# Optimization experiments

Measured on AMD Instinct MI355X. Metric: run time of the kernel, lower is better.

Reference implementation:

```python
import jax, jax.numpy as jnp
import numpy as np

N_ITEM = 100000
DIV_TRADEOFF = 0.1


def setup_inputs() -> dict:
    key = jax.random.key(0)
    ks = jax.random.split(key, 9)
    B, K, L, D_LLM, H = 512, 8, 50, 768, 128
    return {
        "user_id": jax.random.randint(ks[0], (B,), 0, 50000),
        "base_model_preds": jax.random.randint(ks[1], (B, K, L), 0, N_ITEM + 1),
        "preference_in": jax.random.normal(ks[2], (B, H), jnp.float32),
        "pos_label": jax.random.normal(ks[3], (B, K), jnp.float32),
        "neg_label": jax.random.normal(ks[4], (B, K), jnp.float32),
        "user_embeddings": jax.random.normal(ks[5], (50000, H), jnp.float32) * 0.01,
        "item_embeddings": jax.random.normal(ks[6], (N_ITEM + 1, D_LLM), jnp.float32) * 0.02,
        "W_proj": jax.random.normal(ks[7], (D_LLM, H), jnp.float32) * (1.0 / np.sqrt(D_LLM)),
        "b_proj": jax.random.normal(ks[8], (H,), jnp.float32) * 0.01,
    }


def reference(user_id, base_model_preds, preference_in, pos_label, neg_label,
              user_embeddings, item_embeddings, W_proj, b_proj):
    B, K, L = base_model_preds.shape
    # masked gather-embed: ids outside (0, n_item] map to a zero row
    valid = (base_model_preds > 0) & (base_model_preds <= N_ITEM)
    safe_ids = jnp.where(valid, base_model_preds, 0)
    focus_llm = item_embeddings[safe_ids] * valid[..., None].astype(item_embeddings.dtype)  # [B,K,L,D_llm]
    # linear projection to hidden (bias applied everywhere, matching nn.Linear on zeroed rows)
    bm = jnp.einsum('bkld,dh->bklh', focus_llm, W_proj) + b_proj  # [B,K,L,H]
    # time-decay weighted sum over sequence positions
    time_w = 1.0 / jnp.log2(jnp.arange(L, dtype=jnp.float32) + 2.0)  # [L]
    basemodel_emb = jnp.einsum('bklh,l->bkh', bm, time_w)  # [B,K,H]
    # preference = DIEN(...) + user_emb  (DIEN output modeled by preference_in)
    preference = preference_in + user_embeddings[user_id]  # [B,H]
    wgts_org = jnp.einsum('bkh,bh->bk', basemodel_emb, preference)
    wgts = jax.nn.softmax(wgts_org, axis=-1)  # [B,K]
    pos_scores = jnp.sum(pos_label * wgts, axis=1)
    neg_scores = jnp.sum(neg_label * wgts, axis=1)
    loss = -jnp.sum(jax.nn.log_sigmoid(pos_scores - neg_scores))
    # diversity regularizer (use_div=True)
    cov_wgt = jax.lax.stop_gradient(wgts[:, None, :] + wgts[:, :, None])  # [B,K,K]
    cov_mask = 1.0 - jnp.eye(K, dtype=wgts.dtype)  # [K,K]
    gram = jnp.einsum('bih,bjh->bij', basemodel_emb, basemodel_emb) ** 2
    loss_div = DIV_TRADEOFF * jnp.mean(cov_mask[None] * gram * cov_wgt)
    return loss + loss_div
```

## Files before the change

### kernel.cpp

```cpp
#include <hip/hip_runtime.h>
#include <math.h>

#define B_SZ 512
#define K_SZ 8
#define L_SZ 50
#define DLLM 768
#define H_SZ 128
#define N_ITEM 100000
#define DIV_TRADEOFF 0.1f
#define M_PAD 100032

typedef float  f32x4 __attribute__((ext_vector_type(4)));
typedef short  bf16x8 __attribute__((ext_vector_type(8)));
typedef unsigned int u32x4 __attribute__((ext_vector_type(4)));
typedef unsigned short u16x8 __attribute__((ext_vector_type(8)));

__device__ __forceinline__ unsigned short f2bf(float f) {
    unsigned u = __float_as_uint(f);
    u += 0x7fffu + ((u >> 16) & 1u);
    return (unsigned short)(u >> 16);
}

__device__ __forceinline__ void gload_lds16(const void* g, void* l) {
    __builtin_amdgcn_global_load_lds(
        (const __attribute__((address_space(1))) unsigned*)g,
        (__attribute__((address_space(3))) unsigned*)l, 16, 0, 0);
}

__global__ __launch_bounds__(256) void k_wt(
    const float* __restrict__ W,
    unsigned short* __restrict__ Wt,
    float* __restrict__ out)
{
    __shared__ float tile[64][65];
    const int kb = blockIdx.x >> 1;
    const int nb = blockIdx.x & 1;
    const int t  = threadIdx.x;
    if (blockIdx.x == 0 && t == 0) out[0] = 0.0f;

    const int r  = t >> 2;
    const int c0 = (t & 3) * 16;
    #pragma unroll
    for (int j = 0; j < 4; ++j) {
        const float4 v = *(const float4*)(W + (size_t)(kb * 64 + r) * H_SZ + nb * 64 + c0 + j * 4);
        tile[r][c0 + j * 4 + 0] = v.x;
        tile[r][c0 + j * 4 + 1] = v.y;
        tile[r][c0 + j * 4 + 2] = v.z;
        tile[r][c0 + j * 4 + 3] = v.w;
    }
    __syncthreads();
    const int n  = t >> 2;
    const int k0 = (t & 3) * 16;
    u16x8 lo, hi;
    #pragma unroll
    for (int j = 0; j < 8; ++j) lo[j] = f2bf(tile[k0 + j][n]);
    #pragma unroll
    for (int j = 0; j < 8; ++j) hi[j] = f2bf(tile[k0 + 8 + j][n]);
    unsigned short* dst = Wt + (size_t)(nb * 64 + n) * DLLM + kb * 64 + k0;
    *(u16x8*)(dst)     = lo;
    *(u16x8*)(dst + 8) = hi;
}

__global__ __launch_bounds__(256) void k_proj(
    const float* __restrict__ item,
    const unsigned short* __restrict__ Wt,
    float* __restrict__ proj)
{
    __shared__ float          As[64 * 64];
    __shared__ unsigned short Bs[128 * 64];

    const int t    = threadIdx.x;
    const int brow = blockIdx.x * 64;
    const int w    = t >> 6;
    const int lane = t & 63;
    const int nl   = lane & 15;
    const int g    = lane >> 4;
    const int key  = nl & 7;

    const int a_rsub = (lane >> 4);
    const int a_gl   = lane & 15;
    const int b_nsub = (lane >> 3);
    const int b_gl   = lane & 7;
    const int b_key  = b_nsub & 7;

    const int r = w * 16 + nl;

    f32x4 acc[8];
    #pragma unroll
    for (int i = 0; i < 8; ++i) acc[i] = (f32x4){0.f, 0.f, 0.f, 0.f};

    for (int c = 0; c < 12; ++c) {
        const int kc = c * 64;

        #pragma unroll
        for (int i = 0; i < 4; ++i) {
            const int row_t = w * 16 + i * 4 + a_rsub;
            const int rowS  = (brow + row_t <= N_ITEM) ? (brow + row_t) : N_ITEM;
            const int ka    = (a_gl ^ (row_t & 7)) * 4;
            gload_lds16(item + (size_t)rowS * DLLM + kc + ka,
                        &As[w * 1024 + i * 256]);
        }
        #pragma unroll
        for (int i = 0; i < 4; ++i) {
            const int n_t = w * 32 + i * 8 + b_nsub;
            const int kb  = (b_gl ^ b_key) * 8;
            gload_lds16(Wt + (size_t)n_t * DLLM + kc + kb,
                        &Bs[w * 2048 + i * 512]);
        }
        __syncthreads();

        #pragma unroll
        for (int ks = 0; ks < 2; ++ks) {
            const f32x4 alo = *(const f32x4*)&As[r * 64 + 4 * ((ks * 8 + 2 * g)     ^ key)];
            const f32x4 ahi = *(const f32x4*)&As[r * 64 + 4 * ((ks * 8 + 2 * g + 1) ^ key)];
            unsigned p0, p1, p2, p3;
            asm("v_cvt_pk_bf16_f32 %0, %1, %2" : "=v"(p0) : "v"(alo.x), "v"(alo.y));
            asm("v_cvt_pk_bf16_f32 %0, %1, %2" : "=v"(p1) : "v"(alo.z), "v"(alo.w));
            asm("v_cvt_pk_bf16_f32 %0, %1, %2" : "=v"(p2) : "v"(ahi.x), "v"(ahi.y));
            asm("v_cvt_pk_bf16_f32 %0, %1, %2" : "=v"(p3) : "v"(ahi.z), "v"(ahi.w));
            union { u32x4 u; bf16x8 s; } af;
            af.u[0] = p0; af.u[1] = p1; af.u[2] = p2; af.u[3] = p3;

            #pragma unroll
            for (int nt = 0; nt < 8; ++nt) {
                const bf16x8 b = *(const bf16x8*)&Bs[(nt * 16 + nl) * 64
                                                     + 8 * ((ks * 4 + g) ^ key)];
                acc[nt] = __builtin_amdgcn_mfma_f32_16x16x32_bf16(af.s, b, acc[nt], 0, 0, 0);
            }
        }
        __syncthreads();
    }

    const int rbase = brow + w * 16 + 4 * g;
    #pragma unroll
    for (int nt = 0; nt < 8; ++nt) {
        #pragma unroll
        for (int rr = 0; rr < 4; ++rr) {
            proj[(size_t)(rbase + rr) * H_SZ + nt * 16 + nl] = acc[nt][rr];
        }
    }
}

__global__ __launch_bounds__(256) void k_gather2(
    const int* __restrict__ preds,
    const float* __restrict__ proj,
    const float* __restrict__ bproj,
    float* __restrict__ emb)
{
    const int tid = threadIdx.x;
    const int sub = tid >> 7;
    const int h   = tid & 127;
    const int bk  = blockIdx.x * 2 + sub;
    const int* __restrict__ p = preds + (size_t)bk * L_SZ;

    constexpr int PF = 8;
    float buf[PF], wgt[PF];
    #pragma unroll
    for (int i = 0; i < PF; ++i) {
        const int id = p[i];
        const bool v = (id > 0) && (id <= N_ITEM);
        wgt[i] = v ? (1.0f / log2f((float)(i + 2))) : 0.0f;
        buf[i] = proj[(size_t)(v ? id : 0) * H_SZ + h];
    }
    float acc = 0.f;
    #pragma unroll
    for (int l = 0; l < L_SZ; ++l) {
        const int s = l % PF;
        acc += wgt[s] * buf[s];
        if (l + PF < L_SZ) {
            const int id = p[l + PF];
            const bool v = (id > 0) && (id <= N_ITEM);
            wgt[s] = v ? (1.0f / log2f((float)(l + PF + 2))) : 0.0f;
            buf[s] = proj[(size_t)(v ? id : 0) * H_SZ + h];
        }
    }
    float sumw = 0.f;
    #pragma unroll
    for (int l = 0; l < L_SZ; ++l) sumw += 1.0f / log2f((float)(l + 2));
    emb[(size_t)bk * H_SZ + h] = acc + bproj[h] * sumw;
}

__global__ __launch_bounds__(256) void k_loss(
    const int* __restrict__ user_id, const float* __restrict__ pref_in,
    const float* __restrict__ pos_label, const float* __restrict__ neg_label,
    const float* __restrict__ user_emb, const float* __restrict__ emb,
    float* __restrict__ out)
{
    const int b = blockIdx.x;
    const int tid = threadIdx.x;
    __shared__ float pref[H_SZ];
    __shared__ float e[K_SZ][H_SZ + 1];
    __shared__ float sdot[K_SZ];
    __shared__ float wg[K_SZ];
    __shared__ float lossb_s;
    if (tid < H_SZ) {
        const int uid = user_id[b];
        pref[tid] = pref_in[(size_t)b * H_SZ + tid] + user_emb[(size_t)uid * H_SZ + tid];
    }
    const float* eb = emb + (size_t)b * K_SZ * H_SZ;
    #pragma unroll
    for (int i = 0; i < 4; ++i) {
        const int idx = tid * 4 + i;
        e[idx >> 7][idx & (H_SZ - 1)] = eb[idx];
    }
    __syncthreads();
    {
        const int k = tid >> 5;
        const int lane = tid & 31;
        float s = e[k][lane] * pref[lane] + e[k][lane + 32] * pref[lane + 32]
                + e[k][lane + 64] * pref[lane + 64] + e[k][lane + 96] * pref[lane + 96];
        #pragma unroll
        for (int m = 16; m >= 1; m >>= 1) s += __shfl_xor(s, m, 64);
        if (lane == 0) sdot[k] = s;
    }
    __syncthreads();
    if (tid == 0) {
        float mx = sdot[0];
        #pragma unroll
        for (int k = 1; k < K_SZ; ++k) mx = fmaxf(mx, sdot[k]);
        float sum = 0.f; float ex[K_SZ];
        #pragma unroll
        for (int k = 0; k < K_SZ; ++k) { ex[k] = expf(sdot[k] - mx); sum += ex[k]; }
        float ps = 0.f, ns = 0.f;
        #pragma unroll
        for (int k = 0; k < K_SZ; ++k) {
            const float w = ex[k] / sum;
            wg[k] = w;
            ps += pos_label[(size_t)b * K_SZ + k] * w;
            ns += neg_label[(size_t)b * K_SZ + k] * w;
        }
        const float x = ps - ns;
        lossb_s = fmaxf(-x, 0.f) + log1pf(expf(-fabsf(x)));
    }
    __syncthreads();
    if (tid < 64) {
        const int i = tid >> 3;
        const int j = tid & 7;
        float g = 0.f;
        for (int h = 0; h < H_SZ; ++h) g += e[i][h] * e[j][h];
        float v = (i != j) ? (g * g * (wg[i] + wg[j])) : 0.f;
        #pragma unroll
        for (int m = 32; m >= 1; m >>= 1) v += __shfl_xor(v, m, 64);
        if (tid == 0) {
            const float mean_div = v / (float)(B_SZ * K_SZ * K_SZ);
            atomicAdd(out, lossb_s + DIV_TRADEOFF * mean_div);
        }
    }
}

__global__ __launch_bounds__(192) void k_gather_fb(
    const int* __restrict__ preds, const float* __restrict__ item,
    float* __restrict__ wf, float* __restrict__ out)
{
    const int bk  = blockIdx.x;
    const int tid = threadIdx.x;
    if (bk == 0 && tid == 0) out[0] = 0.0f;
    const int* __restrict__ p = preds + (size_t)bk * L_SZ;
    const float* __restrict__ ibase = item + (size_t)tid * 4;
    float4 acc = make_float4(0.f, 0.f, 0.f, 0.f);
    constexpr int PF = 8;
    float4 buf[PF]; float wgt[PF];
    #pragma unroll
    for (int i = 0; i < PF; ++i) {
        const int id = p[i];
        const bool v = (id > 0) && (id <= N_ITEM);
        wgt[i] = v ? (1.0f / log2f((float)(i + 2))) : 0.0f;
        buf[i] = *(const float4*)(ibase + (size_t)(v ? id : 0) * DLLM);
    }
    #pragma unroll
    for (int l = 0; l < L_SZ; ++l) {
        const int s = l % PF;
        const float4 v4 = buf[s];
        const float  w  = wgt[s];
        if (l + PF < L_SZ) {
            const int id = p[l + PF];
            const bool v = (id > 0) && (id <= N_ITEM);
            wgt[s] = v ? (1.0f / log2f((float)(l + PF + 2))) : 0.0f;
            buf[s] = *(const float4*)(ibase + (size_t)(v ? id : 0) * DLLM);
        }
        acc.x += w * v4.x; acc.y += w * v4.y; acc.z += w * v4.z; acc.w += w * v4.w;
    }
    *(float4*)(wf + (size_t)bk * DLLM + (size_t)tid * 4) = acc;
}

__global__ __launch_bounds__(256) void k_projloss_fb(
    const float* __restrict__ wf, const float* __restrict__ W,
    const float* __restrict__ bproj, const int* __restrict__ user_id,
    const float* __restrict__ pref_in, const float* __restrict__ pos_label,
    const float* __restrict__ neg_label, const float* __restrict__ user_emb,
    float* __restrict__ out)
{
    const int b   = blockIdx.x;
    const int tid = threadIdx.x;
    const int c   = tid & (H_SZ - 1);
    const int rg  = tid >> 7;
    __shared__ float A[K_SZ][H_SZ];
    __shared__ float e[K_SZ][H_SZ + 1];
    __shared__ float pref[H_SZ];
    __shared__ float sdot[K_SZ];
    __shared__ float wg[K_SZ];
    __shared__ float lossb_s;
    float acc[4] = {0.f, 0.f, 0.f, 0.f};
    const size_t rowbase = (size_t)b * K_SZ;
    for (int kb = 0; kb < DLLM; kb += H_SZ) {
        __syncthreads();
        {
            const int r  = tid >> 5;
            const int kk = (tid & 31) * 4;
            *(float4*)&A[r][kk] = *(const float4*)(wf + (rowbase + r) * DLLM + kb + kk);
        }
        __syncthreads();
        #pragma unroll 4
        for (int k = 0; k < H_SZ; k += 4) {
            const float4 a0 = *(const float4*)&A[rg][k];
            const float4 a1 = *(const float4*)&A[rg + 2][k];
            const float4 a2 = *(const float4*)&A[rg + 4][k];
            const float4 a3 = *(const float4*)&A[rg + 6][k];
            const float* Wp = W + (size_t)(kb + k) * H_SZ + c;
            const float w0 = Wp[0]; const float w1 = Wp[H_SZ];
            const float w2 = Wp[2 * H_SZ]; const float w3 = Wp[3 * H_SZ];
            acc[0] += a0.x * w0 + a0.y * w1 + a0.z * w2 + a0.w * w3;
            acc[1] += a1.x * w0 + a1.y * w1 + a1.z * w2 + a1.w * w3;
            acc[2] += a2.x * w0 + a2.y * w1 + a2.z * w2 + a2.w * w3;
            acc[3] += a3.x * w0 + a3.y * w1 + a3.z * w2 + a3.w * w3;
        }
    }
    float sumw = 0.f;
    #pragma unroll
    for (int l = 0; l < L_SZ; ++l) sumw += 1.0f / log2f((float)(l + 2));
    const float bterm = bproj[c] * sumw;
    #pragma unroll
    for (int ri = 0; ri < 4; ++ri) e[rg + 2 * ri][c] = acc[ri] + bterm;
    if (tid < H_SZ) {
        const int uid = user_id[b];
        pref[tid] = pref_in[(size_t)b * H_SZ + tid] + user_emb[(size_t)uid * H_SZ + tid];
    }
    __syncthreads();
    {
        const int k    = tid >> 5;
        const int lane = tid & 31;
        float s = e[k][lane] * pref[lane] + e[k][lane + 32] * pref[lane + 32]
                + e[k][lane + 64] * pref[lane + 64] + e[k][lane + 96] * pref[lane + 96];
        #pragma unroll
        for (int m = 16; m >= 1; m >>= 1) s += __shfl_xor(s, m, 64);
        if (lane == 0) sdot[k] = s;
    }
    __syncthreads();
    if (tid == 0) {
        float mx = sdot[0];
        #pragma unroll
        for (int k = 1; k < K_SZ; ++k) mx = fmaxf(mx, sdot[k]);
        float sum = 0.f; float ex[K_SZ];
        #pragma unroll
        for (int k = 0; k < K_SZ; ++k) { ex[k] = expf(sdot[k] - mx); sum += ex[k]; }
        float ps = 0.f, ns = 0.f;
        #pragma unroll
        for (int k = 0; k < K_SZ; ++k) {
            const float w = ex[k] / sum;
            wg[k] = w;
            ps += pos_label[(size_t)b * K_SZ + k] * w;
            ns += neg_label[(size_t)b * K_SZ + k] * w;
        }
        const float x = ps - ns;
        lossb_s = fmaxf(-x, 0.f) + log1pf(expf(-fabsf(x)));
    }
    __syncthreads();
    if (tid < 64) {
        const int i = tid >> 3;
        const int j = tid & 7;
        float g = 0.f;
        for (int h = 0; h < H_SZ; ++h) g += e[i][h] * e[j][h];
        float v = (i != j) ? (g * g * (wg[i] + wg[j])) : 0.f;
        #pragma unroll
        for (int m = 32; m >= 1; m >>= 1) v += __shfl_xor(v, m, 64);
        if (tid == 0) {
            const float mean_div = v / (float)(B_SZ * K_SZ * K_SZ);
            atomicAdd(out, lossb_s + DIV_TRADEOFF * mean_div);
        }
    }
}

extern "C" void kernel_launch(void* const* d_in, const int* in_sizes, int n_in,
                              void* d_out, int out_size, void* d_ws, size_t ws_size,
                              hipStream_t stream) {
    const int*   user_id   = (const int*)  d_in[0];
    const int*   preds     = (const int*)  d_in[1];
    const float* pref_in   = (const float*)d_in[2];
    const float* pos_label = (const float*)d_in[3];
    const float* neg_label = (const float*)d_in[4];
    const float* user_emb  = (const float*)d_in[5];
    const float* item_emb  = (const float*)d_in[6];
    const float* W_proj    = (const float*)d_in[7];
    const float* b_proj    = (const float*)d_in[8];

    float* out = (float*)d_out;

    const size_t proj_bytes = (size_t)M_PAD * H_SZ * sizeof(float);
    const size_t wt_off     = proj_bytes;
    const size_t wt_bytes   = (size_t)H_SZ * DLLM * sizeof(unsigned short);
    const size_t emb_off    = wt_off + wt_bytes;
    const size_t emb_bytes  = (size_t)B_SZ * K_SZ * H_SZ * sizeof(float);
    const size_t need       = emb_off + emb_bytes;

    if (ws_size >= need) {
        float*          proj = (float*)d_ws;
        unsigned short* Wt   = (unsigned short*)((char*)d_ws + wt_off);
        float*          emb  = (float*)((char*)d_ws + emb_off);

        k_wt<<<24, 256, 0, stream>>>(W_proj, Wt, out);
        k_proj<<<M_PAD / 64, 256, 0, stream>>>(item_emb, Wt, proj);
        k_gather2<<<B_SZ * K_SZ / 2, 256, 0, stream>>>(preds, proj, b_proj, emb);
        k_loss<<<B_SZ, 256, 0, stream>>>(user_id, pref_in, pos_label, neg_label,
                                         user_emb, emb, out);
    } else {
        float* wf = (float*)d_ws;
        k_gather_fb<<<B_SZ * K_SZ, 192, 0, stream>>>(preds, item_emb, wf, out);
        k_projloss_fb<<<B_SZ, 256, 0, stream>>>(wf, W_proj, b_proj, user_id, pref_in,
                                                pos_label, neg_label, user_emb, out);
    }
}
```

Baseline: 116.7 us.

## Double-buffer k_proj LDS staging and store projected items as bf16

The projection GEMM now double-buffers its A/B LDS tiles, prefetching the next K chunk with direct-to-LDS loads while MFMAs run on the current one, using explicit vmcnt waits and raw barriers. The projected table is written as bf16 instead of fp32, halving its write and the gather's read traffic. The gather kernel is reorganized so each wavefront handles one (b,k) row and reads two bf16 values per lane. This adds bf16 rounding error to the projected embeddings and doubles LDS use per block, which may lower occupancy.

```diff
diff --git a/kernel.cpp b/kernel.cpp
--- a/kernel.cpp
+++ b/kernel.cpp
@@ -64,10 +64,10 @@
 __global__ __launch_bounds__(256) void k_proj(
     const float* __restrict__ item,
     const unsigned short* __restrict__ Wt,
-    float* __restrict__ proj)
-{
-    __shared__ float          As[64 * 64];
-    __shared__ unsigned short Bs[128 * 64];
+    unsigned short* __restrict__ projb)
+{
+    __shared__ float          As[2][64 * 64];
+    __shared__ unsigned short Bs[2][128 * 64];
 
     const int t    = threadIdx.x;
     const int brow = blockIdx.x * 64;
@@ -85,34 +85,43 @@
 
     const int r = w * 16 + nl;
 
-    f32x4 acc[8];
-    #pragma unroll
-    for (int i = 0; i < 8; ++i) acc[i] = (f32x4){0.f, 0.f, 0.f, 0.f};
-
-    for (int c = 0; c < 12; ++c) {
+    auto STAGE = [&](int d, int c) {
         const int kc = c * 64;
-
         #pragma unroll
         for (int i = 0; i < 4; ++i) {
             const int row_t = w * 16 + i * 4 + a_rsub;
             const int rowS  = (brow + row_t <= N_ITEM) ? (brow + row_t) : N_ITEM;
             const int ka    = (a_gl ^ (row_t & 7)) * 4;
             gload_lds16(item + (size_t)rowS * DLLM + kc + ka,
-                        &As[w * 1024 + i * 256]);
+                        &As[d][w * 1024 + i * 256]);
         }
         #pragma unroll
         for (int i = 0; i < 4; ++i) {
             const int n_t = w * 32 + i * 8 + b_nsub;
             const int kb  = (b_gl ^ b_key) * 8;
             gload_lds16(Wt + (size_t)n_t * DLLM + kc + kb,
-                        &Bs[w * 2048 + i * 512]);
-        }
-        __syncthreads();
+                        &Bs[d][w * 2048 + i * 512]);
+        }
+    };
+
+    f32x4 acc[8];
+    #pragma unroll
+    for (int i = 0; i < 8; ++i) acc[i] = (f32x4){0.f, 0.f, 0.f, 0.f};
+
+    STAGE(0, 0);
+
+    for (int c = 0; c < 12; ++c) {
+        const int cur = c & 1;
+        if (c < 11) STAGE(cur ^ 1, c + 1);
+        if (c < 11) asm volatile("s_waitcnt vmcnt(8)" ::: "memory");
+        else        asm volatile("s_waitcnt vmcnt(0)" ::: "memory");
+        __builtin_amdgcn_s_barrier();
+        __builtin_amdgcn_sched_barrier(0);
 
         #pragma unroll
         for (int ks = 0; ks < 2; ++ks) {
-            const f32x4 alo = *(const f32x4*)&As[r * 64 + 4 * ((ks * 8 + 2 * g)     ^ key)];
-            const f32x4 ahi = *(const f32x4*)&As[r * 64 + 4 * ((ks * 8 + 2 * g + 1) ^ key)];
+            const f32x4 alo = *(const f32x4*)&As[cur][r * 64 + 4 * ((ks * 8 + 2 * g)     ^ key)];
+            const f32x4 ahi = *(const f32x4*)&As[cur][r * 64 + 4 * ((ks * 8 + 2 * g + 1) ^ key)];
             unsigned p0, p1, p2, p3;
             asm("v_cvt_pk_bf16_f32 %0, %1, %2" : "=v"(p0) : "v"(alo.x), "v"(alo.y));
             asm("v_cvt_pk_bf16_f32 %0, %1, %2" : "=v"(p1) : "v"(alo.z), "v"(alo.w));
@@ -123,12 +132,14 @@
 
             #pragma unroll
             for (int nt = 0; nt < 8; ++nt) {
-                const bf16x8 b = *(const bf16x8*)&Bs[(nt * 16 + nl) * 64
-                                                     + 8 * ((ks * 4 + g) ^ key)];
+                const bf16x8 b = *(const bf16x8*)&Bs[cur][(nt * 16 + nl) * 64
+                                                          + 8 * ((ks * 4 + g) ^ key)];
                 acc[nt] = __builtin_amdgcn_mfma_f32_16x16x32_bf16(af.s, b, acc[nt], 0, 0, 0);
             }
         }
-        __syncthreads();
+        asm volatile("s_waitcnt lgkmcnt(0)" ::: "memory");
+        __builtin_amdgcn_s_barrier();
+        __builtin_amdgcn_sched_barrier(0);
     }
 
     const int rbase = brow + w * 16 + 4 * g;
@@ -136,48 +147,55 @@
     for (int nt = 0; nt < 8; ++nt) {
         #pragma unroll
         for (int rr = 0; rr < 4; ++rr) {
-            proj[(size_t)(rbase + rr) * H_SZ + nt * 16 + nl] = acc[nt][rr];
+            projb[(size_t)(rbase + rr) * H_SZ + nt * 16 + nl] = f2bf(acc[nt][rr]);
         }
     }
 }
 
 __global__ __launch_bounds__(256) void k_gather2(
     const int* __restrict__ preds,
-    const float* __restrict__ proj,
+    const unsigned short* __restrict__ projb,
     const float* __restrict__ bproj,
     float* __restrict__ emb)
 {
-    const int tid = threadIdx.x;
-    const int sub = tid >> 7;
-    const int h   = tid & 127;
-    const int bk  = blockIdx.x * 2 + sub;
+    const int wv   = threadIdx.x >> 6;
+    const int lane = threadIdx.x & 63;
+    const int bk   = blockIdx.x * 4 + wv;
+    const int h2   = lane * 2;
     const int* __restrict__ p = preds + (size_t)bk * L_SZ;
 
     constexpr int PF = 8;
-    float buf[PF], wgt[PF];
+    unsigned buf[PF];
+    float wgt[PF];
     #pragma unroll
     for (int i = 0; i < PF; ++i) {
         const int id = p[i];
         const bool v = (id > 0) && (id <= N_ITEM);
         wgt[i] = v ? (1.0f / log2f((float)(i + 2))) : 0.0f;
-        buf[i] = proj[(size_t)(v ? id : 0) * H_SZ + h];
-    }
-    float acc = 0.f;
+        buf[i] = *(const unsigned*)(projb + (size_t)(v ? id : 0) * H_SZ + h2);
+    }
+    float a0 = 0.f, a1 = 0.f;
     #pragma unroll
     for (int l = 0; l < L_SZ; ++l) {
         const int s = l % PF;
-        acc += wgt[s] * buf[s];
+        const unsigned u = buf[s];
+        const float w = wgt[s];
         if (l + PF < L_SZ) {
             const int id = p[l + PF];
             const bool v = (id > 0) && (id <= N_ITEM);
             wgt[s] = v ? (1.0f / log2f((float)(l + PF + 2))) : 0.0f;
-            buf[s] = proj[(size_t)(v ? id : 0) * H_SZ + h];
-        }
+            buf[s] = *(const unsigned*)(projb + (size_t)(v ? id : 0) * H_SZ + h2);
+        }
+        a0 += w * __uint_as_float(u << 16);
+        a1 += w * __uint_as_float(u & 0xffff0000u);
     }
     float sumw = 0.f;
     #pragma unroll
     for (int l = 0; l < L_SZ; ++l) sumw += 1.0f / log2f((float)(l + 2));
-    emb[(size_t)bk * H_SZ + h] = acc + bproj[h] * sumw;
+    float2 o;
+    o.x = a0 + bproj[h2]     * sumw;
+    o.y = a1 + bproj[h2 + 1] * sumw;
+    *(float2*)(emb + (size_t)bk * H_SZ + h2) = o;
 }
 
 __global__ __launch_bounds__(256) void k_loss(
@@ -395,21 +413,21 @@
 
     float* out = (float*)d_out;
 
-    const size_t proj_bytes = (size_t)M_PAD * H_SZ * sizeof(float);
-    const size_t wt_off     = proj_bytes;
-    const size_t wt_bytes   = (size_t)H_SZ * DLLM * sizeof(unsigned short);
-    const size_t emb_off    = wt_off + wt_bytes;
-    const size_t emb_bytes  = (size_t)B_SZ * K_SZ * H_SZ * sizeof(float);
-    const size_t need       = emb_off + emb_bytes;
+    const size_t projb_bytes = (size_t)M_PAD * H_SZ * sizeof(unsigned short);
+    const size_t wt_off      = projb_bytes;
+    const size_t wt_bytes    = (size_t)H_SZ * DLLM * sizeof(unsigned short);
+    const size_t emb_off     = wt_off + wt_bytes;
+    const size_t emb_bytes   = (size_t)B_SZ * K_SZ * H_SZ * sizeof(float);
+    const size_t need        = emb_off + emb_bytes;
 
     if (ws_size >= need) {
-        float*          proj = (float*)d_ws;
-        unsigned short* Wt   = (unsigned short*)((char*)d_ws + wt_off);
-        float*          emb  = (float*)((char*)d_ws + emb_off);
+        unsigned short* projb = (unsigned short*)d_ws;
+        unsigned short* Wt    = (unsigned short*)((char*)d_ws + wt_off);
+        float*          emb   = (float*)((char*)d_ws + emb_off);
 
         k_wt<<<24, 256, 0, stream>>>(W_proj, Wt, out);
-        k_proj<<<M_PAD / 64, 256, 0, stream>>>(item_emb, Wt, proj);
-        k_gather2<<<B_SZ * K_SZ / 2, 256, 0, stream>>>(preds, proj, b_proj, emb);
+        k_proj<<<M_PAD / 64, 256, 0, stream>>>(item_emb, Wt, projb);
+        k_gather2<<<B_SZ * K_SZ / 4, 256, 0, stream>>>(preds, projb, b_proj, emb);
         k_loss<<<B_SZ, 256, 0, stream>>>(user_id, pref_in, pos_label, neg_label,
                                          user_emb, emb, out);
     } else {
```

Result: faster. 107.8 us (-7.6%).
